# Kernel tuning notes

Hardware: AMD Instinct MI355X
Metric: run time of the kernel (lower is better)

## Reference

```python
import jax, jax.numpy as jnp
import numpy as np

C = 64  # channel dim fixed by Conv1D filters=64 and residual add

def setup_inputs() -> dict:
    key = jax.random.key(0)
    kF, kM, kN, kV = jax.random.split(key, 4)
    B, T = 8, 2048
    F = jax.random.normal(kF, (B, T, C), dtype=jnp.float32)
    # Conv1D(kernel_size=1, use_bias=False) == pointwise dense: weight [C_in, filters]
    scale = 1.0 / np.sqrt(C)
    W_M = jax.random.normal(kM, (C, C), dtype=jnp.float32) * scale
    W_N = jax.random.normal(kN, (C, C), dtype=jnp.float32) * scale
    W_V = jax.random.normal(kV, (C, C), dtype=jnp.float32) * scale
    return {"F": F, "W_M": W_M, "W_N": W_N, "W_V": W_V}

def reference(F, W_M, W_N, W_V):
    # 1x1 conv projections (pointwise matmul over channel dim)
    M = jnp.einsum('btc,cd->btd', F, W_M)  # Q
    N = jnp.einsum('btc,cd->btd', F, W_N)  # K
    V = jnp.einsum('btc,cd->btd', F, W_V)
    # correlation = Q @ K^T ; softmax over last axis (keras Softmax default)
    scores = jnp.einsum('bqd,bkd->bqk', M, N)  # [B, T, T]
    S = jax.nn.softmax(scores, axis=-1)
    out = jnp.einsum('bqk,bkd->bqd', S, V)
    return out + F  # residual
```

## Files before the change

### kernel.cpp

```cpp
#include <hip/hip_runtime.h>
#include <hip/hip_bf16.h>

#define B_ 8
#define T_ 2048
#define LOG2E 1.4426950408889634f

typedef _Float16 half8 __attribute__((ext_vector_type(8)));
typedef _Float16 half4 __attribute__((ext_vector_type(4)));
typedef float f32x4 __attribute__((ext_vector_type(4)));

#define MFMA16(A, Bv, Cv) __builtin_amdgcn_mfma_f32_16x16x32_f16((A), (Bv), (Cv), 0, 0, 0)

__device__ inline float xexp2(float x)
{
    float r;
    asm("v_exp_f32 %0, %1" : "=v"(r) : "v"(x));
    return r;
}

__global__ __launch_bounds__(256) void prepack_kernel(
    const float* __restrict__ WM, const float* __restrict__ WN,
    const float* __restrict__ WV, _Float16* __restrict__ Wp)
{
    const int idx = blockIdx.x * 256 + threadIdx.x;
    const int m = idx >> 12;
    const int r = idx & 4095;
    const int d = r >> 6;
    const int k = r & 63;
    const float* W = (m == 0) ? WM : (m == 1) ? WN : WV;
    Wp[m * 4096 + d * 64 + k] = (_Float16)W[k * 64 + d];
}

__global__ __launch_bounds__(256) void proj_kernel(
    const float* __restrict__ F, const _Float16* __restrict__ Wp,
    _Float16* __restrict__ Qf, _Float16* __restrict__ Kf,
    _Float16* __restrict__ Vf)
{
    const int lane = threadIdx.x & 63;
    const int dt   = threadIdx.x >> 6;
    const int ql = lane & 15;
    const int g  = lane >> 4;
    const int blk = blockIdx.x;
    const int b   = blk & 7;
    const int rt  = blk >> 3;
    const int rowbase = b * T_ + rt * 16;

    const float* fr = F + (size_t)(rowbase + ql) * 64;
    const f32x4 v00 = *(const f32x4*)(fr + 8 * g);
    const f32x4 v01 = *(const f32x4*)(fr + 8 * g + 4);
    const f32x4 v10 = *(const f32x4*)(fr + 32 + 8 * g);
    const f32x4 v11 = *(const f32x4*)(fr + 32 + 8 * g + 4);
    half8 af0, af1;
#pragma unroll
    for (int j = 0; j < 4; ++j) {
        af0[j]     = (_Float16)v00[j];
        af0[4 + j] = (_Float16)v01[j];
        af1[j]     = (_Float16)v10[j];
        af1[4 + j] = (_Float16)v11[j];
    }

    const half8* wq = (const half8*)(Wp);
    const half8* wk = (const half8*)(Wp + 4096);
    const half8* wv = (const half8*)(Wp + 8192);

    const int fi = (dt * 16 + ql) * 8;
    f32x4 z = {0.f, 0.f, 0.f, 0.f};
    f32x4 accQ = MFMA16(wq[fi + g], af0, z);
    accQ = MFMA16(wq[fi + 4 + g], af1, accQ);
    f32x4 accK = MFMA16(wk[fi + g], af0, z);
    accK = MFMA16(wk[fi + 4 + g], af1, accK);
    f32x4 accV = MFMA16(af0, wv[fi + g], z);
    accV = MFMA16(af1, wv[fi + 4 + g], accV);

    const int d0 = dt * 16 + 4 * g;
    const int p  = ((d0 >> 5) << 2) | ((d0 >> 3) & 3);
    const size_t tbase = (((size_t)b * 128 + rt) * 8 + p) * 128 + ql * 8 + (d0 & 7);
    {
        half4 qs;
#pragma unroll
        for (int r = 0; r < 4; ++r) qs[r] = (_Float16)(accQ[r] * LOG2E);
        *(half4*)(Qf + tbase) = qs;
    }
    {
        half4 ks;
#pragma unroll
        for (int r = 0; r < 4; ++r) ks[r] = (_Float16)accK[r];
        *(half4*)(Kf + tbase) = ks;
    }
    {
        half4 vs;
#pragma unroll
        for (int r = 0; r < 4; ++r) vs[r] = (_Float16)accV[r];
        const int kt5 = rt >> 1;
        const int cp0 = 8 * g + 4 * (rt & 1);
        *(half4*)(Vf + ((((size_t)b * 64 + kt5) * 4 + dt) * 16 + ql) * 32 + cp0) = vs;
    }
}

#define PROC(qf0, qf1, a0, a1, a2, a3, mr, ls)                               \
    do {                                                                     \
        f32x4 s0 = {0.f, 0.f, 0.f, 0.f};                                     \
        f32x4 s1 = {0.f, 0.f, 0.f, 0.f};                                     \
        s0 = MFMA16(k0lo, qf0, s0);                                          \
        s0 = MFMA16(k0hi, qf1, s0);                                          \
        s1 = MFMA16(k1lo, qf0, s1);                                          \
        s1 = MFMA16(k1hi, qf1, s1);                                          \
        const float p0 = s0[0], p1 = s0[1], p2 = s0[2], p3 = s0[3];          \
        const float p4 = s1[0], p5 = s1[1], p6 = s1[2], p7 = s1[3];          \
        const float q0_ = fmaxf(fmaxf(p0, p1), p2);                          \
        const float q1_ = fmaxf(fmaxf(p3, p4), p5);                          \
        const float q2_ = fmaxf(fmaxf(p6, p7), q0_);                         \
        const float pm  = fmaxf(q1_, q2_);                                   \
        if (__any(pm - mr > 8.0f)) {                                         \
            float pmw = fmaxf(pm, __shfl_xor(pm, 16));                       \
            pmw = fmaxf(pmw, __shfl_xor(pmw, 32));                           \
            const float mnew = fmaxf(mr, pmw);                               \
            const float fac  = xexp2(mr - mnew);                             \
            mr = mnew;                                                       \
            ls *= fac;                                                       \
            const int lg = 4 * ((threadIdx.x & 63) >> 4);                    \
            const int lb = (threadIdx.x & 48);                               \
            const float f0 = __shfl(fac, lb | (lg + 0));                     \
            const float f1 = __shfl(fac, lb | (lg + 1));                     \
            const float f2 = __shfl(fac, lb | (lg + 2));                     \
            const float f3 = __shfl(fac, lb | (lg + 3));                     \
            a0[0] *= f0; a0[1] *= f1; a0[2] *= f2; a0[3] *= f3;              \
            a1[0] *= f0; a1[1] *= f1; a1[2] *= f2; a1[3] *= f3;              \
            a2[0] *= f0; a2[1] *= f1; a2[2] *= f2; a2[3] *= f3;              \
            a3[0] *= f0; a3[1] *= f1; a3[2] *= f2; a3[3] *= f3;              \
        }                                                                    \
        const float e0 = xexp2(p0 - mr), e1 = xexp2(p1 - mr);                \
        const float e2 = xexp2(p2 - mr), e3 = xexp2(p3 - mr);                \
        const float e4 = xexp2(p4 - mr), e5 = xexp2(p5 - mr);                \
        const float e6 = xexp2(p6 - mr), e7 = xexp2(p7 - mr);                \
        ls += ((e0 + e1) + (e2 + e3)) + ((e4 + e5) + (e6 + e7));             \
        half8 pav;                                                           \
        pav[0] = (_Float16)e0; pav[1] = (_Float16)e1;                        \
        pav[2] = (_Float16)e2; pav[3] = (_Float16)e3;                        \
        pav[4] = (_Float16)e4; pav[5] = (_Float16)e5;                        \
        pav[6] = (_Float16)e6; pav[7] = (_Float16)e7;                        \
        a0 = MFMA16(pav, v0, a0);                                            \
        a1 = MFMA16(pav, v1, a1);                                            \
        a2 = MFMA16(pav, v2, a2);                                            \
        a3 = MFMA16(pav, v3, a3);                                            \
    } while (0)

__global__ __launch_bounds__(512, 1) void attn_kernel(
    const _Float16* __restrict__ Qf, const _Float16* __restrict__ Kf,
    const _Float16* __restrict__ Vf, const float* __restrict__ F,
    float* __restrict__ out)
{
    __shared__ float Ol[8][64][68];
    __shared__ float Ml[8][64];
    __shared__ float Ll[8][64];

    const int lane = threadIdx.x & 63;
    const int wid  = threadIdx.x >> 6;
    const int blk  = blockIdx.x;
    const int b    = blk & 7;
    const int tile = blk >> 3;
    const int ql = lane & 15;
    const int g  = lane >> 4;

    const half8* QfB = (const half8*)Qf + (size_t)b * 16384;
    const half8* KfB = (const half8*)Kf + (size_t)b * 16384;
    const half8* VfB = (const half8*)Vf + (size_t)b * 16384;

    const half8* qtA = QfB + (size_t)(4 * tile + 0) * 128;
    const half8* qtB = QfB + (size_t)(4 * tile + 1) * 128;
    const half8* qtC = QfB + (size_t)(4 * tile + 2) * 128;
    const half8* qtD = QfB + (size_t)(4 * tile + 3) * 128;
    const half8 qA0 = qtA[g * 16 + ql], qA1 = qtA[(4 + g) * 16 + ql];
    const half8 qB0 = qtB[g * 16 + ql], qB1 = qtB[(4 + g) * 16 + ql];
    const half8 qC0 = qtC[g * 16 + ql], qC1 = qtC[(4 + g) * 16 + ql];
    const half8 qD0 = qtD[g * 16 + ql], qD1 = qtD[(4 + g) * 16 + ql];

    const f32x4 z4 = {0.f, 0.f, 0.f, 0.f};
    f32x4 aA0 = z4, aA1 = z4, aA2 = z4, aA3 = z4;
    f32x4 aB0 = z4, aB1 = z4, aB2 = z4, aB3 = z4;
    f32x4 aC0 = z4, aC1 = z4, aC2 = z4, aC3 = z4;
    f32x4 aD0 = z4, aD1 = z4, aD2 = z4, aD3 = z4;
    float mA = -1e30f, lsA = 0.f;
    float mB = -1e30f, lsB = 0.f;
    float mC = -1e30f, lsC = 0.f;
    float mD = -1e30f, lsD = 0.f;

    const int kb0 = wid << 8;
    const half8* kA = KfB + (size_t)(kb0 >> 4) * 128 + g * 16 + ql;
    const half8* vA = VfB + (size_t)(kb0 >> 5) * 256 + ql * 4 + g;

    half8 k0lo = kA[0];
    half8 k0hi = kA[64];
    half8 k1lo = kA[128];
    half8 k1hi = kA[192];
    half8 v0 = vA[0];
    half8 v1 = vA[64];
    half8 v2 = vA[128];
    half8 v3 = vA[192];

    for (int it = 0; it < 8; ++it) {
        half8 nk0lo, nk0hi, nk1lo, nk1hi, nv0, nv1, nv2, nv3;
        if (it < 7) {
            nk0lo = kA[256];
            nk0hi = kA[256 + 64];
            nk1lo = kA[256 + 128];
            nk1hi = kA[256 + 192];
            nv0 = vA[256];
            nv1 = vA[256 + 64];
            nv2 = vA[256 + 128];
            nv3 = vA[256 + 192];
        }

        PROC(qA0, qA1, aA0, aA1, aA2, aA3, mA, lsA);
        PROC(qB0, qB1, aB0, aB1, aB2, aB3, mB, lsB);
        PROC(qC0, qC1, aC0, aC1, aC2, aC3, mC, lsC);
        PROC(qD0, qD1, aD0, aD1, aD2, aD3, mD, lsD);

        if (it < 7) {
            k0lo = nk0lo; k0hi = nk0hi; k1lo = nk1lo; k1hi = nk1hi;
            v0 = nv0; v1 = nv1; v2 = nv2; v3 = nv3;
        }
        kA += 256;
        vA += 256;
    }

    lsA += __shfl_xor(lsA, 16); lsA += __shfl_xor(lsA, 32);
    lsB += __shfl_xor(lsB, 16); lsB += __shfl_xor(lsB, 32);
    lsC += __shfl_xor(lsC, 16); lsC += __shfl_xor(lsC, 32);
    lsD += __shfl_xor(lsD, 16); lsD += __shfl_xor(lsD, 32);

#pragma unroll
    for (int r = 0; r < 4; ++r) {
        Ol[wid][     4 * g + r][ 0 + ql] = aA0[r];
        Ol[wid][     4 * g + r][16 + ql] = aA1[r];
        Ol[wid][     4 * g + r][32 + ql] = aA2[r];
        Ol[wid][     4 * g + r][48 + ql] = aA3[r];
        Ol[wid][16 + 4 * g + r][ 0 + ql] = aB0[r];
        Ol[wid][16 + 4 * g + r][16 + ql] = aB1[r];
        Ol[wid][16 + 4 * g + r][32 + ql] = aB2[r];
        Ol[wid][16 + 4 * g + r][48 + ql] = aB3[r];
        Ol[wid][32 + 4 * g + r][ 0 + ql] = aC0[r];
        Ol[wid][32 + 4 * g + r][16 + ql] = aC1[r];
        Ol[wid][32 + 4 * g + r][32 + ql] = aC2[r];
        Ol[wid][32 + 4 * g + r][48 + ql] = aC3[r];
        Ol[wid][48 + 4 * g + r][ 0 + ql] = aD0[r];
        Ol[wid][48 + 4 * g + r][16 + ql] = aD1[r];
        Ol[wid][48 + 4 * g + r][32 + ql] = aD2[r];
        Ol[wid][48 + 4 * g + r][48 + ql] = aD3[r];
    }
    if (g == 0) {
        Ml[wid][     ql] = mA;  Ll[wid][     ql] = lsA;
        Ml[wid][16 + ql] = mB;  Ll[wid][16 + ql] = lsB;
        Ml[wid][32 + ql] = mC;  Ll[wid][32 + ql] = lsC;
        Ml[wid][48 + ql] = mD;  Ll[wid][48 + ql] = lsD;
    }
    __syncthreads();

    const int tid = threadIdx.x;
    const int qq  = tid >> 3;
    const int d0  = (tid & 7) * 8;

    float mm[8], lv[8];
#pragma unroll
    for (int s = 0; s < 8; ++s) {
        mm[s] = Ml[s][qq];
        lv[s] = Ll[s][qq];
    }
    float ms = mm[0];
#pragma unroll
    for (int s = 1; s < 8; ++s) ms = fmaxf(ms, mm[s]);
    float lt = 0.f;
    f32x4 oa = {0.f, 0.f, 0.f, 0.f};
    f32x4 ob2 = {0.f, 0.f, 0.f, 0.f};
#pragma unroll
    for (int s = 0; s < 8; ++s) {
        const float sc = xexp2(mm[s] - ms);
        lt += lv[s] * sc;
        oa  += *(const f32x4*)(&Ol[s][qq][d0])     * sc;
        ob2 += *(const f32x4*)(&Ol[s][qq][d0 + 4]) * sc;
    }
    const float inv = 1.0f / lt;
    const size_t grow = (size_t)b * T_ + (tile << 6) + qq;
    const f32x4 fr0 = *(const f32x4*)(F + grow * 64 + d0);
    const f32x4 fr1 = *(const f32x4*)(F + grow * 64 + d0 + 4);
    *(f32x4*)(out + grow * 64 + d0)     = oa * inv + fr0;
    *(f32x4*)(out + grow * 64 + d0 + 4) = ob2 * inv + fr1;
}

extern "C" void kernel_launch(void* const* d_in, const int* in_sizes, int n_in,
                              void* d_out, int out_size, void* d_ws, size_t ws_size,
                              hipStream_t stream)
{
    const float* F  = (const float*)d_in[0];
    const float* WM = (const float*)d_in[1];
    const float* WN = (const float*)d_in[2];
    const float* WV = (const float*)d_in[3];
    float* out = (float*)d_out;

    const size_t proj_bytes = (size_t)B_ * T_ * 64 * sizeof(_Float16);
    char* ws = (char*)d_ws;
    _Float16* Qf = (_Float16*)(ws);
    _Float16* Kf = (_Float16*)(ws + proj_bytes);
    _Float16* Vf = (_Float16*)(ws + 2 * proj_bytes);
    _Float16* Wp = (_Float16*)(ws + 3 * proj_bytes);

    hipLaunchKernelGGL(prepack_kernel, dim3(48), dim3(256), 0, stream,
                       WM, WN, WV, Wp);
    hipLaunchKernelGGL(proj_kernel, dim3(B_ * T_ / 16), dim3(256), 0, stream,
                       F, Wp, Qf, Kf, Vf);
    hipLaunchKernelGGL(attn_kernel, dim3(B_ * T_ / 64), dim3(512), 0, stream,
                       Qf, Kf, Vf, F, out);
}
```

Measured before the change: 32.43 us.

## Fuse weight prepack into projection and batch score MFMAs before softmax

```diff
diff --git a/kernel.cpp b/kernel.cpp
--- a/kernel.cpp
+++ b/kernel.cpp
@@ -18,21 +18,9 @@
     return r;
 }
 
-__global__ __launch_bounds__(256) void prepack_kernel(
-    const float* __restrict__ WM, const float* __restrict__ WN,
-    const float* __restrict__ WV, _Float16* __restrict__ Wp)
-{
-    const int idx = blockIdx.x * 256 + threadIdx.x;
-    const int m = idx >> 12;
-    const int r = idx & 4095;
-    const int d = r >> 6;
-    const int k = r & 63;
-    const float* W = (m == 0) ? WM : (m == 1) ? WN : WV;
-    Wp[m * 4096 + d * 64 + k] = (_Float16)W[k * 64 + d];
-}
-
 __global__ __launch_bounds__(256) void proj_kernel(
-    const float* __restrict__ F, const _Float16* __restrict__ Wp,
+    const float* __restrict__ F, const float* __restrict__ WM,
+    const float* __restrict__ WN, const float* __restrict__ WV,
     _Float16* __restrict__ Qf, _Float16* __restrict__ Kf,
     _Float16* __restrict__ Vf)
 {
@@ -44,6 +32,7 @@
     const int b   = blk & 7;
     const int rt  = blk >> 3;
     const int rowbase = b * T_ + rt * 16;
+    const int d = dt * 16 + ql;
 
     const float* fr = F + (size_t)(rowbase + ql) * 64;
     const f32x4 v00 = *(const f32x4*)(fr + 8 * g);
@@ -59,18 +48,26 @@
         af1[4 + j] = (_Float16)v11[j];
     }
 
-    const half8* wq = (const half8*)(Wp);
-    const half8* wk = (const half8*)(Wp + 4096);
-    const half8* wv = (const half8*)(Wp + 8192);
-
-    const int fi = (dt * 16 + ql) * 8;
+    half8 wq0, wq1, wk0, wk1, wv0, wv1;
+#pragma unroll
+    for (int j = 0; j < 8; ++j) {
+        const int k0 = (8 * g + j) * 64 + d;
+        const int k1 = (32 + 8 * g + j) * 64 + d;
+        wq0[j] = (_Float16)WM[k0];
+        wq1[j] = (_Float16)WM[k1];
+        wk0[j] = (_Float16)WN[k0];
+        wk1[j] = (_Float16)WN[k1];
+        wv0[j] = (_Float16)WV[k0];
+        wv1[j] = (_Float16)WV[k1];
+    }
+
     f32x4 z = {0.f, 0.f, 0.f, 0.f};
-    f32x4 accQ = MFMA16(wq[fi + g], af0, z);
-    accQ = MFMA16(wq[fi + 4 + g], af1, accQ);
-    f32x4 accK = MFMA16(wk[fi + g], af0, z);
-    accK = MFMA16(wk[fi + 4 + g], af1, accK);
-    f32x4 accV = MFMA16(af0, wv[fi + g], z);
-    accV = MFMA16(af1, wv[fi + 4 + g], accV);
+    f32x4 accQ = MFMA16(wq0, af0, z);
+    accQ = MFMA16(wq1, af1, accQ);
+    f32x4 accK = MFMA16(wk0, af0, z);
+    accK = MFMA16(wk1, af1, accK);
+    f32x4 accV = MFMA16(af0, wv0, z);
+    accV = MFMA16(af1, wv1, accV);
 
     const int d0 = dt * 16 + 4 * g;
     const int p  = ((d0 >> 5) << 2) | ((d0 >> 3) & 3);
@@ -97,14 +94,8 @@
     }
 }
 
-#define PROC(qf0, qf1, a0, a1, a2, a3, mr, ls)                               \
+#define SM(s0, s1, a0, a1, a2, a3, mr, ls)                                   \
     do {                                                                     \
-        f32x4 s0 = {0.f, 0.f, 0.f, 0.f};                                     \
-        f32x4 s1 = {0.f, 0.f, 0.f, 0.f};                                     \
-        s0 = MFMA16(k0lo, qf0, s0);                                          \
-        s0 = MFMA16(k0hi, qf1, s0);                                          \
-        s1 = MFMA16(k1lo, qf0, s1);                                          \
-        s1 = MFMA16(k1hi, qf1, s1);                                          \
         const float p0 = s0[0], p1 = s0[1], p2 = s0[2], p3 = s0[3];          \
         const float p4 = s1[0], p5 = s1[1], p6 = s1[2], p7 = s1[3];          \
         const float q0_ = fmaxf(fmaxf(p0, p1), p2);                          \
@@ -211,10 +202,29 @@
             nv3 = vA[256 + 192];
         }
 
-        PROC(qA0, qA1, aA0, aA1, aA2, aA3, mA, lsA);
-        PROC(qB0, qB1, aB0, aB1, aB2, aB3, mB, lsB);
-        PROC(qC0, qC1, aC0, aC1, aC2, aC3, mC, lsC);
-        PROC(qD0, qD1, aD0, aD1, aD2, aD3, mD, lsD);
+        f32x4 sA0 = z4, sA1 = z4, sB0 = z4, sB1 = z4;
+        f32x4 sC0 = z4, sC1 = z4, sD0 = z4, sD1 = z4;
+        sA0 = MFMA16(k0lo, qA0, sA0);
+        sB0 = MFMA16(k0lo, qB0, sB0);
+        sC0 = MFMA16(k0lo, qC0, sC0);
+        sD0 = MFMA16(k0lo, qD0, sD0);
+        sA1 = MFMA16(k1lo, qA0, sA1);
+        sB1 = MFMA16(k1lo, qB0, sB1);
+        sC1 = MFMA16(k1lo, qC0, sC1);
+        sD1 = MFMA16(k1lo, qD0, sD1);
+        sA0 = MFMA16(k0hi, qA1, sA0);
+        sB0 = MFMA16(k0hi, qB1, sB0);
+        sC0 = MFMA16(k0hi, qC1, sC0);
+        sD0 = MFMA16(k0hi, qD1, sD0);
+        sA1 = MFMA16(k1hi, qA1, sA1);
+        sB1 = MFMA16(k1hi, qB1, sB1);
+        sC1 = MFMA16(k1hi, qC1, sC1);
+        sD1 = MFMA16(k1hi, qD1, sD1);
+
+        SM(sA0, sA1, aA0, aA1, aA2, aA3, mA, lsA);
+        SM(sB0, sB1, aB0, aB1, aB2, aB3, mB, lsB);
+        SM(sC0, sC1, aC0, aC1, aC2, aC3, mC, lsC);
+        SM(sD0, sD1, aD0, aD1, aD2, aD3, mD, lsD);
 
         if (it < 7) {
             k0lo = nk0lo; k0hi = nk0hi; k1lo = nk1lo; k1hi = nk1hi;
@@ -302,12 +312,9 @@
     _Float16* Qf = (_Float16*)(ws);
     _Float16* Kf = (_Float16*)(ws + proj_bytes);
     _Float16* Vf = (_Float16*)(ws + 2 * proj_bytes);
-    _Float16* Wp = (_Float16*)(ws + 3 * proj_bytes);
-
-    hipLaunchKernelGGL(prepack_kernel, dim3(48), dim3(256), 0, stream,
-                       WM, WN, WV, Wp);
+
     hipLaunchKernelGGL(proj_kernel, dim3(B_ * T_ / 16), dim3(256), 0, stream,
-                       F, Wp, Qf, Kf, Vf);
+                       F, WM, WN, WV, Qf, Kf, Vf);
     hipLaunchKernelGGL(attn_kernel, dim3(B_ * T_ / 64), dim3(512), 0, stream,
                        Qf, Kf, Vf, F, out);
 }
```

Measured after the change: 26.41 us. 18.6% less time.
